# Kernel tuning notes

Measured on AMD Instinct MI355X. Metric: run time of the kernel, lower is better.

## Reference

```python
import jax, jax.numpy as jnp
import numpy as np

B, DIM, H, HD, DS = 256, 1024, 16, 64, 4
NL, NKV = HD, HD * DS  # mask shape constraint: num_tok_q == head_dim, num_tok_kv == head_dim*downscaling
EPS = 1e-5


def _ln(t, g, b):
    m = t.mean(-1, keepdims=True)
    v = ((t - m) ** 2).mean(-1, keepdims=True)
    return (t - m) / jnp.sqrt(v + EPS) * g + b


def setup_inputs() -> dict:
    key = jax.random.key(0)
    ks = jax.random.split(key, 7)
    s = DIM ** -0.5
    return {
        'x': jax.random.normal(ks[0], (B, NKV, DIM), jnp.float32),
        'latents': jax.random.normal(ks[1], (B, NL, DIM), jnp.float32),
        'Wq': jax.random.normal(ks[2], (DIM, DIM), jnp.float32) * s,
        'Wk': jax.random.normal(ks[3], (DIM, DIM), jnp.float32) * s,
        'Wv': jax.random.normal(ks[4], (DIM, DIM), jnp.float32) * s,
        'Wo': jax.random.normal(ks[5], (DIM, DIM), jnp.float32) * s,
        'bo': jnp.zeros((DIM,), jnp.float32),
        'g_out': jnp.ones((DIM,), jnp.float32),
        'b_out': jnp.zeros((DIM,), jnp.float32),
        'g_x': jnp.ones((DIM,), jnp.float32),
        'b_x': jnp.zeros((DIM,), jnp.float32),
        'g_l': jnp.ones((DIM,), jnp.float32),
        'b_l': jnp.zeros((DIM,), jnp.float32),
    }


def reference(x, latents, Wq, Wk, Wv, Wo, bo, g_out, b_out, g_x, b_x, g_l, b_l):
    # pre-norms
    ln_l = _ln(latents, g_l, b_l)   # (B, NL, DIM) -> queries
    ln_x = _ln(x, g_x, b_x)         # (B, NKV, DIM) -> keys/values
    # QKV projections (torch Linear: y = x @ W.T), split heads: b n (h d) -> b h n d
    q = (ln_l @ Wq.T).reshape(B, NL, H, HD).transpose(0, 2, 1, 3)
    k = (ln_x @ Wk.T).reshape(B, NKV, H, HD).transpose(0, 2, 1, 3)
    v = (ln_x @ Wv.T).reshape(B, NKV, H, HD).transpose(0, 2, 1, 3)
    qk = jnp.einsum('bhid,bhjd->bhij', q, k) * (HD ** -0.5)  # (B,H,NL,NKV)
    # faithful to original: (HD,HD) strict-upper -inf mask, repeat_interleave by DS along kv axis
    mask = jnp.triu(jnp.full((HD, HD), -jnp.inf, jnp.float32), k=1)
    mask = jnp.repeat(mask, DS, axis=1)  # (NL, NKV)
    attn = jax.nn.softmax(qk + mask[None, None], axis=-1)
    out = jnp.einsum('bhij,bhjd->bhid', attn, v)
    out = out.transpose(0, 2, 1, 3).reshape(B, NL, DIM)  # b h n d -> b n (h d)
    out = _ln(out, g_out, b_out)      # norm_out (hard-coded True)
    out = out @ Wo.T + bo             # to_out; dropout p=0 -> identity
    return latents + out              # residual=True
```

## Files before the change

### kernel.cpp

```cpp
#include <hip/hip_runtime.h>


typedef unsigned short u16;
typedef float f32x4 __attribute__((ext_vector_type(4)));
typedef short bf16x8 __attribute__((ext_vector_type(8)));
typedef u16 u16x4 __attribute__((ext_vector_type(4)));

#define DEV __device__ __forceinline__

DEV u16 f2bf(float f) {
  union { float f; unsigned int u; } c; c.f = f;
  unsigned int u = c.u;
  u += 0x7fffu + ((u >> 16) & 1u);
  return (u16)(u >> 16);
}
DEV float bf2f(u16 u) {
  union { unsigned int u; float f; } c; c.u = ((unsigned int)u) << 16; return c.f;
}
DEV f32x4 mfma16(bf16x8 a, bf16x8 b, f32x4 c) {
  return __builtin_amdgcn_mfma_f32_16x16x32_bf16(a, b, c, 0, 0, 0);
}
DEV void gl16(const void* g, void* l) {
  __builtin_amdgcn_global_load_lds((const __attribute__((address_space(1))) void*)g,
                                   (__attribute__((address_space(3))) void*)l, 16, 0, 0);
}

template<int INBF>
__global__ __launch_bounds__(256) void ln_kernel(const void* __restrict__ src,
                                                 const float* __restrict__ g,
                                                 const float* __restrict__ bta,
                                                 u16* __restrict__ dst) {
  const int row = blockIdx.x, tid = threadIdx.x;
  float v[4];
  if constexpr (INBF) {
    const u16x4 r = *((const u16x4*)((const u16*)src + (size_t)row * 1024) + tid);
#pragma unroll
    for (int i = 0; i < 4; ++i) v[i] = bf2f(r[i]);
  } else {
    const float4 r = *((const float4*)((const float*)src + (size_t)row * 1024) + tid);
    v[0] = r.x; v[1] = r.y; v[2] = r.z; v[3] = r.w;
  }
  float s = v[0] + v[1] + v[2] + v[3];
  float q = v[0]*v[0] + v[1]*v[1] + v[2]*v[2] + v[3]*v[3];
#pragma unroll
  for (int off = 32; off; off >>= 1) {
    s += __shfl_xor(s, off, 64);
    q += __shfl_xor(q, off, 64);
  }
  __shared__ float red[8];
  if ((tid & 63) == 0) { red[(tid >> 6) * 2] = s; red[(tid >> 6) * 2 + 1] = q; }
  __syncthreads();
  s = red[0] + red[2] + red[4] + red[6];
  q = red[1] + red[3] + red[5] + red[7];
  const float mean = s * (1.f / 1024.f);
  const float rstd = rsqrtf(q * (1.f / 1024.f) - mean * mean + 1e-5f);
  const float4 gv = *((const float4*)g + tid);
  const float4 bv = *((const float4*)bta + tid);
  u16x4 o;
  o[0] = f2bf((v[0] - mean) * rstd * gv.x + bv.x);
  o[1] = f2bf((v[1] - mean) * rstd * gv.y + bv.y);
  o[2] = f2bf((v[2] - mean) * rstd * gv.z + bv.z);
  o[3] = f2bf((v[3] - mean) * rstd * gv.w + bv.w);
  *((u16x4*)(dst + (size_t)row * 1024) + tid) = o;
}

__global__ __launch_bounds__(256) void cvt4_kernel(const float* __restrict__ w0,
                                                   const float* __restrict__ w1,
                                                   const float* __restrict__ w2,
                                                   const float* __restrict__ w3,
                                                   u16* __restrict__ out) {
  const int g = blockIdx.x >> 10;
  const float* src = (g == 0) ? w0 : (g == 1) ? w1 : (g == 2) ? w2 : w3;
  const int i = ((blockIdx.x & 1023) * 256 + threadIdx.x) * 4;
  const float4 v = *(const float4*)(src + i);
  u16x4 o; o[0] = f2bf(v.x); o[1] = f2bf(v.y); o[2] = f2bf(v.z); o[3] = f2bf(v.w);
  *(u16x4*)(out + (size_t)g * 1048576 + i) = o;
}

template<int MODE>
__global__ __launch_bounds__(512, 2) void gemm256(const u16* __restrict__ A,
                                                  const u16* __restrict__ B0,
                                                  const u16* __restrict__ B1,
                                                  u16* __restrict__ o0,
                                                  u16* __restrict__ o1,
                                                  const float* __restrict__ bias,
                                                  const float* __restrict__ resid,
                                                  float* __restrict__ outf,
                                                  int tiles_n) {
  constexpr int NT = 16;
  __shared__ u16 As[2][16384];
  __shared__ u16 Bs[2][16384];
  const int tid = threadIdx.x, lane = tid & 63, wid = tid >> 6;
  const int wm = wid >> 2, wn = wid & 3;
  const int q8 = (int)gridDim.x >> 3;
  const int wg = ((int)blockIdx.x & 7) * q8 + ((int)blockIdx.x >> 3);
  const int tn = wg % tiles_n, tm = wg / tiles_n;

  const u16* Asrc = A + (size_t)tm * 256 * 1024;
  const u16* Bsrc;
  if constexpr (MODE == 0)
    Bsrc = (tn < 4) ? (B0 + (size_t)tn * 256 * 1024) : (B1 + (size_t)(tn - 4) * 256 * 1024);
  else
    Bsrc = B0 + (size_t)tn * 256 * 1024;

  int goff[4], loff[4];
#pragma unroll
  for (int i = 0; i < 4; ++i) {
    const int s = i * 512 + tid;
    const int gr = s >> 3, gc = (s & 7) ^ (gr & 7);
    goff[i] = gr * 1024 + gc * 8;
    loff[i] = s * 8;
  }
  const int fr = lane & 15, fq = lane >> 4;
  int chk[2];
#pragma unroll
  for (int ks = 0; ks < 2; ++ks) chk[ks] = ((((ks << 2) + fq)) ^ (lane & 7)) * 8;

  f32x4 acc[8][4];
  const f32x4 z = {0.f, 0.f, 0.f, 0.f};
#pragma unroll
  for (int m = 0; m < 8; ++m)
#pragma unroll
    for (int n = 0; n < 4; ++n) acc[m][n] = z;

#define STG_A(buf, kt, h) { gl16(Asrc + (size_t)(kt) * 64 + goff[2*(h)],     &As[buf][loff[2*(h)]]); \
                            gl16(Asrc + (size_t)(kt) * 64 + goff[2*(h)+1],   &As[buf][loff[2*(h)+1]]); }
#define STG_B(buf, kt, h) { gl16(Bsrc + (size_t)(kt) * 64 + goff[2*(h)],     &Bs[buf][loff[2*(h)]]); \
                            gl16(Bsrc + (size_t)(kt) * 64 + goff[2*(h)+1],   &Bs[buf][loff[2*(h)+1]]); }
#define LDA(H) _Pragma("unroll") for (int mp = 0; mp < 4; ++mp) \
               _Pragma("unroll") for (int ks = 0; ks < 2; ++ks) \
                 af[mp][ks] = *(const bf16x8*)&Ab[(wm * 128 + ((H)*4 + mp) * 16 + fr) * 64 + chk[ks]];
#define LDB(DST, G) _Pragma("unroll") for (int np = 0; np < 2; ++np) \
                    _Pragma("unroll") for (int ks = 0; ks < 2; ++ks) \
                      DST[np][ks] = *(const bf16x8*)&Bb[(wn * 64 + ((G)*2 + np) * 16 + fr) * 64 + chk[ks]];
#define MFMA_Q(H, BF, G) _Pragma("unroll") for (int mp = 0; mp < 4; ++mp) \
                         _Pragma("unroll") for (int np = 0; np < 2; ++np) \
                         _Pragma("unroll") for (int ks = 0; ks < 2; ++ks) \
                           acc[(H)*4 + mp][(G)*2 + np] = mfma16(af[mp][ks], BF[np][ks], acc[(H)*4 + mp][(G)*2 + np]);

  STG_A(0, 0, 0); STG_A(0, 0, 1);
  STG_B(0, 0, 0); STG_B(0, 0, 1);
  STG_A(1, 1, 0); STG_A(1, 1, 1);
  asm volatile("s_waitcnt vmcnt(4)" ::: "memory");
  __builtin_amdgcn_s_barrier();

  for (int t = 0; t < NT; ++t) {
    const int bsel = t & 1;
    const u16* Ab = As[bsel];
    const u16* Bb = Bs[bsel];
    bf16x8 af[4][2], bfrA[2][2], bfrB[2][2];
    LDA(0); LDB(bfrA, 0);
    if (t + 1 < NT) STG_B(bsel ^ 1, t + 1, 0);
    __builtin_amdgcn_s_barrier();
    asm volatile("s_waitcnt lgkmcnt(0)" ::: "memory");
    __builtin_amdgcn_s_setprio(1);
    MFMA_Q(0, bfrA, 0);
    __builtin_amdgcn_s_setprio(0);
    __builtin_amdgcn_s_barrier();
    LDB(bfrB, 1);
    if (t + 1 < NT) STG_B(bsel ^ 1, t + 1, 1);
    __builtin_amdgcn_s_barrier();
    asm volatile("s_waitcnt lgkmcnt(0)" ::: "memory");
    __builtin_amdgcn_s_setprio(1);
    MFMA_Q(0, bfrB, 1);
    __builtin_amdgcn_s_setprio(0);
    __builtin_amdgcn_s_barrier();
    LDA(1);
    __builtin_amdgcn_s_barrier();
    asm volatile("s_waitcnt lgkmcnt(0)" ::: "memory");
    __builtin_amdgcn_s_setprio(1);
    MFMA_Q(1, bfrB, 1);
    __builtin_amdgcn_s_setprio(0);
    __builtin_amdgcn_s_barrier();
    if (t + 2 < NT) { STG_A(bsel, t + 2, 0); STG_A(bsel, t + 2, 1); }
    __builtin_amdgcn_s_setprio(1);
    MFMA_Q(1, bfrA, 0);
    __builtin_amdgcn_s_setprio(0);
    if (t + 2 < NT) asm volatile("s_waitcnt vmcnt(4)" ::: "memory");
    else            asm volatile("s_waitcnt vmcnt(0)" ::: "memory");
    __builtin_amdgcn_s_barrier();
  }
#undef STG_A
#undef STG_B
#undef LDA
#undef LDB
#undef MFMA_Q

  if constexpr (MODE == 0) {
    if (tn < 4) {
#pragma unroll
      for (int m = 0; m < 8; ++m) {
        const int t0 = wm * 128 + m * 16 + fq * 4;
#pragma unroll
        for (int n = 0; n < 4; ++n) {
          const int c = tn * 256 + wn * 64 + n * 16 + fr;
          const int h = c >> 6, d = c & 63;
          u16* p = o0 + ((size_t)(tm * 16 + h) * 256 + t0) * 64 + d;
#pragma unroll
          for (int j = 0; j < 4; ++j) p[j * 64] = f2bf(acc[m][n][j]);
        }
      }
    } else {
#pragma unroll
      for (int m = 0; m < 8; ++m) {
        const int t0 = wm * 128 + m * 16 + fq * 4;
#pragma unroll
        for (int n = 0; n < 4; ++n) {
          const int c = (tn - 4) * 256 + wn * 64 + n * 16 + fr;
          const int h = c >> 6, d = c & 63;
          u16x4 o;
#pragma unroll
          for (int j = 0; j < 4; ++j) o[j] = f2bf(acc[m][n][j]);
          *(u16x4*)(o1 + ((size_t)(tm * 16 + h) * 64 + d) * 256 + t0) = o;
        }
      }
    }
  } else if constexpr (MODE == 1) {
#pragma unroll
    for (int m = 0; m < 8; ++m) {
      const int r0 = tm * 256 + wm * 128 + m * 16 + fq * 4;
      const int b = r0 >> 6, i0 = r0 & 63;
#pragma unroll
      for (int n = 0; n < 4; ++n) {
        const int c = tn * 256 + wn * 64 + n * 16 + fr;
        const int h = c >> 6, d = c & 63;
        u16* p = o0 + ((size_t)(b * 16 + h) * 64 + i0) * 64 + d;
#pragma unroll
        for (int j = 0; j < 4; ++j) p[j * 64] = f2bf(acc[m][n][j]);
      }
    }
  } else {
#pragma unroll
    for (int m = 0; m < 8; ++m) {
      const int r0 = tm * 256 + wm * 128 + m * 16 + fq * 4;
#pragma unroll
      for (int n = 0; n < 4; ++n) {
        const int c = tn * 256 + wn * 64 + n * 16 + fr;
        const float bc = bias[c];
#pragma unroll
        for (int j = 0; j < 4; ++j) {
          const size_t idx = (size_t)(r0 + j) * 1024 + c;
          outf[idx] = acc[m][n][j] + bc + resid[idx];
        }
      }
    }
  }
}

__global__ __launch_bounds__(256) void attn_kernel(const u16* __restrict__ Qb,
                                                   const u16* __restrict__ Kb,
                                                   const u16* __restrict__ Vt,
                                                   u16* __restrict__ AO) {
  __shared__ u16 Qs[64 * 64];
  __shared__ u16 Ks[256 * 64];
  __shared__ u16 Vs[64 * 256];
  const int bh = blockIdx.x;
  const int tid = threadIdx.x, lane = tid & 63, wv = tid >> 6;
  const u16* qsrc = Qb + (size_t)bh * 4096;
  const u16* ksrc = Kb + (size_t)bh * 16384;
  const u16* vsrc = Vt + (size_t)bh * 16384;
#pragma unroll
  for (int i = 0; i < 2; ++i) gl16(qsrc + (i * 256 + tid) * 8, &Qs[(i * 256 + tid) * 8]);
#pragma unroll
  for (int i = 0; i < 8; ++i) gl16(ksrc + (i * 256 + tid) * 8, &Ks[(i * 256 + tid) * 8]);
#pragma unroll
  for (int i = 0; i < 8; ++i) gl16(vsrc + (i * 256 + tid) * 8, &Vs[(i * 256 + tid) * 8]);
  __syncthreads();

  f32x4 sacc[16];
  const f32x4 z = {0.f, 0.f, 0.f, 0.f};
#pragma unroll
  for (int n = 0; n < 16; ++n) sacc[n] = z;
#pragma unroll
  for (int s = 0; s < 2; ++s) {
    const bf16x8 aq = *(const bf16x8*)&Qs[(wv * 16 + (lane & 15)) * 64 + s * 32 + (lane >> 4) * 8];
#pragma unroll
    for (int n = 0; n < 16; ++n) {
      const bf16x8 bk = *(const bf16x8*)&Ks[(n * 16 + (lane & 15)) * 64 + s * 32 + (lane >> 4) * 8];
      sacc[n] = mfma16(aq, bk, sacc[n]);
    }
  }

  const int rgrp = lane >> 4, cl = lane & 15;
#pragma unroll
  for (int j = 0; j < 4; ++j) {
    const int qrow = (wv << 4) + (rgrp << 2) + j;
    float m_ = -1e30f;
#pragma unroll
    for (int n = 0; n < 16; ++n) {
      const int col = (n << 4) + cl;
      float sv = sacc[n][j] * 0.125f;
      sv = ((col >> 2) <= qrow) ? sv : -1e30f;
      sacc[n][j] = sv;
      m_ = fmaxf(m_, sv);
    }
#pragma unroll
    for (int off = 8; off; off >>= 1) m_ = fmaxf(m_, __shfl_xor(m_, off, 64));
    float s_ = 0.f;
#pragma unroll
    for (int n = 0; n < 16; ++n) {
      const float p = exp2f((sacc[n][j] - m_) * 1.44269504f);
      sacc[n][j] = p;
      s_ += p;
    }
#pragma unroll
    for (int off = 8; off; off >>= 1) s_ += __shfl_xor(s_, off, 64);
    const float inv = 1.0f / s_;
#pragma unroll
    for (int n = 0; n < 16; ++n) sacc[n][j] *= inv;
  }

  __syncthreads();
  u16* Ps = Ks;
#pragma unroll
  for (int n = 0; n < 16; ++n)
#pragma unroll
    for (int j = 0; j < 4; ++j)
      Ps[((wv << 4) + (rgrp << 2) + j) * 256 + (n << 4) + cl] = f2bf(sacc[n][j]);
  __syncthreads();

  f32x4 oacc[4];
#pragma unroll
  for (int n = 0; n < 4; ++n) oacc[n] = z;
#pragma unroll
  for (int ks = 0; ks < 8; ++ks) {
    const bf16x8 ap = *(const bf16x8*)&Ps[(wv * 16 + (lane & 15)) * 256 + ks * 32 + (lane >> 4) * 8];
#pragma unroll
    for (int n = 0; n < 4; ++n) {
      const bf16x8 bv = *(const bf16x8*)&Vs[(n * 16 + (lane & 15)) * 256 + ks * 32 + (lane >> 4) * 8];
      oacc[n] = mfma16(ap, bv, oacc[n]);
    }
  }
  const int b = bh >> 4, h = bh & 15;
  u16* obase = AO + (size_t)b * 65536 + (size_t)h * 64;
#pragma unroll
  for (int n = 0; n < 4; ++n)
#pragma unroll
    for (int j = 0; j < 4; ++j) {
      const int qrow = (wv << 4) + (rgrp << 2) + j;
      const int d = (n << 4) + cl;
      obase[(size_t)qrow * 1024 + d] = f2bf(oacc[n][j]);
    }
}

extern "C" void kernel_launch(void* const* d_in, const int* in_sizes, int n_in,
                              void* d_out, int out_size, void* d_ws, size_t ws_size,
                              hipStream_t stream) {
  const float* x     = (const float*)d_in[0];
  const float* lat   = (const float*)d_in[1];
  const float* Wq    = (const float*)d_in[2];
  const float* Wk    = (const float*)d_in[3];
  const float* Wv    = (const float*)d_in[4];
  const float* Wo    = (const float*)d_in[5];
  const float* bo    = (const float*)d_in[6];
  const float* g_out = (const float*)d_in[7];
  const float* b_out = (const float*)d_in[8];
  const float* g_x   = (const float*)d_in[9];
  const float* b_x   = (const float*)d_in[10];
  const float* g_l   = (const float*)d_in[11];
  const float* b_l   = (const float*)d_in[12];
  float* out = (float*)d_out;

  char* W = (char*)d_ws;
  u16* wqb = (u16*)(W + 0);
  u16* wkb = (u16*)(W + 2097152);
  u16* wvb = (u16*)(W + 4194304);
  u16* wob = (u16*)(W + 6291456);
  u16* lnl = (u16*)(W + 8388608);
  u16* lnx = (u16*)(W + 41943040);
  u16* qb  = (u16*)(W + 176160768);
  u16* kb  = (u16*)(W + 209715200);
  u16* vt  = (u16*)(W + 343932928);
  u16* ao  = lnx;
  u16* lna = qb;

  cvt4_kernel<<<4096, 256, 0, stream>>>(Wq, Wk, Wv, Wo, wqb);

  ln_kernel<0><<<16384, 256, 0, stream>>>(lat, g_l, b_l, lnl);
  ln_kernel<0><<<65536, 256, 0, stream>>>(x, g_x, b_x, lnx);

  gemm256<0><<<256 * 8, 512, 0, stream>>>(lnx, wkb, wvb, kb, vt, nullptr, nullptr, nullptr, 8);
  gemm256<1><<<64 * 4, 512, 0, stream>>>(lnl, wqb, nullptr, qb, nullptr, nullptr, nullptr, nullptr, 4);

  attn_kernel<<<4096, 256, 0, stream>>>(qb, kb, vt, ao);

  ln_kernel<1><<<16384, 256, 0, stream>>>(ao, g_out, b_out, lna);

  gemm256<2><<<64 * 4, 512, 0, stream>>>(lna, wob, nullptr, nullptr, nullptr, bo, lat, out, 4);
}
```

Before: 649.3 us.

## Replace interleaved 8-wave GEMM schedule with simple double-buffered tile loop

```diff
diff --git a/kernel.cpp b/kernel.cpp
--- a/kernel.cpp
+++ b/kernel.cpp
@@ -123,68 +123,49 @@
 #pragma unroll
     for (int n = 0; n < 4; ++n) acc[m][n] = z;
 
-#define STG_A(buf, kt, h) { gl16(Asrc + (size_t)(kt) * 64 + goff[2*(h)],     &As[buf][loff[2*(h)]]); \
-                            gl16(Asrc + (size_t)(kt) * 64 + goff[2*(h)+1],   &As[buf][loff[2*(h)+1]]); }
-#define STG_B(buf, kt, h) { gl16(Bsrc + (size_t)(kt) * 64 + goff[2*(h)],     &Bs[buf][loff[2*(h)]]); \
-                            gl16(Bsrc + (size_t)(kt) * 64 + goff[2*(h)+1],   &Bs[buf][loff[2*(h)+1]]); }
-#define LDA(H) _Pragma("unroll") for (int mp = 0; mp < 4; ++mp) \
-               _Pragma("unroll") for (int ks = 0; ks < 2; ++ks) \
-                 af[mp][ks] = *(const bf16x8*)&Ab[(wm * 128 + ((H)*4 + mp) * 16 + fr) * 64 + chk[ks]];
-#define LDB(DST, G) _Pragma("unroll") for (int np = 0; np < 2; ++np) \
-                    _Pragma("unroll") for (int ks = 0; ks < 2; ++ks) \
-                      DST[np][ks] = *(const bf16x8*)&Bb[(wn * 64 + ((G)*2 + np) * 16 + fr) * 64 + chk[ks]];
-#define MFMA_Q(H, BF, G) _Pragma("unroll") for (int mp = 0; mp < 4; ++mp) \
-                         _Pragma("unroll") for (int np = 0; np < 2; ++np) \
-                         _Pragma("unroll") for (int ks = 0; ks < 2; ++ks) \
-                           acc[(H)*4 + mp][(G)*2 + np] = mfma16(af[mp][ks], BF[np][ks], acc[(H)*4 + mp][(G)*2 + np]);
-
-  STG_A(0, 0, 0); STG_A(0, 0, 1);
-  STG_B(0, 0, 0); STG_B(0, 0, 1);
-  STG_A(1, 1, 0); STG_A(1, 1, 1);
-  asm volatile("s_waitcnt vmcnt(4)" ::: "memory");
+#define STG_TILE(buf, kt) { \
+    gl16(Asrc + (size_t)(kt) * 64 + goff[0], &As[buf][loff[0]]); \
+    gl16(Asrc + (size_t)(kt) * 64 + goff[1], &As[buf][loff[1]]); \
+    gl16(Asrc + (size_t)(kt) * 64 + goff[2], &As[buf][loff[2]]); \
+    gl16(Asrc + (size_t)(kt) * 64 + goff[3], &As[buf][loff[3]]); \
+    gl16(Bsrc + (size_t)(kt) * 64 + goff[0], &Bs[buf][loff[0]]); \
+    gl16(Bsrc + (size_t)(kt) * 64 + goff[1], &Bs[buf][loff[1]]); \
+    gl16(Bsrc + (size_t)(kt) * 64 + goff[2], &Bs[buf][loff[2]]); \
+    gl16(Bsrc + (size_t)(kt) * 64 + goff[3], &Bs[buf][loff[3]]); }
+
+  STG_TILE(0, 0);
+  asm volatile("s_waitcnt vmcnt(0)" ::: "memory");
   __builtin_amdgcn_s_barrier();
 
   for (int t = 0; t < NT; ++t) {
     const int bsel = t & 1;
     const u16* Ab = As[bsel];
     const u16* Bb = Bs[bsel];
-    bf16x8 af[4][2], bfrA[2][2], bfrB[2][2];
-    LDA(0); LDB(bfrA, 0);
-    if (t + 1 < NT) STG_B(bsel ^ 1, t + 1, 0);
+    if (t + 1 < NT) STG_TILE(bsel ^ 1, t + 1);
+    bf16x8 af[8][2], bfr[4][2];
+#pragma unroll
+    for (int m = 0; m < 8; ++m)
+#pragma unroll
+      for (int ks = 0; ks < 2; ++ks)
+        af[m][ks] = *(const bf16x8*)&Ab[(wm * 128 + m * 16 + fr) * 64 + chk[ks]];
+#pragma unroll
+    for (int n = 0; n < 4; ++n)
+#pragma unroll
+      for (int ks = 0; ks < 2; ++ks)
+        bfr[n][ks] = *(const bf16x8*)&Bb[(wn * 64 + n * 16 + fr) * 64 + chk[ks]];
+    __builtin_amdgcn_s_setprio(1);
+#pragma unroll
+    for (int m = 0; m < 8; ++m)
+#pragma unroll
+      for (int n = 0; n < 4; ++n)
+#pragma unroll
+        for (int ks = 0; ks < 2; ++ks)
+          acc[m][n] = mfma16(af[m][ks], bfr[n][ks], acc[m][n]);
+    __builtin_amdgcn_s_setprio(0);
+    asm volatile("s_waitcnt vmcnt(0)" ::: "memory");
     __builtin_amdgcn_s_barrier();
-    asm volatile("s_waitcnt lgkmcnt(0)" ::: "memory");
-    __builtin_amdgcn_s_setprio(1);
-    MFMA_Q(0, bfrA, 0);
-    __builtin_amdgcn_s_setprio(0);
-    __builtin_amdgcn_s_barrier();
-    LDB(bfrB, 1);
-    if (t + 1 < NT) STG_B(bsel ^ 1, t + 1, 1);
-    __builtin_amdgcn_s_barrier();
-    asm volatile("s_waitcnt lgkmcnt(0)" ::: "memory");
-    __builtin_amdgcn_s_setprio(1);
-    MFMA_Q(0, bfrB, 1);
-    __builtin_amdgcn_s_setprio(0);
-    __builtin_amdgcn_s_barrier();
-    LDA(1);
-    __builtin_amdgcn_s_barrier();
-    asm volatile("s_waitcnt lgkmcnt(0)" ::: "memory");
-    __builtin_amdgcn_s_setprio(1);
-    MFMA_Q(1, bfrB, 1);
-    __builtin_amdgcn_s_setprio(0);
-    __builtin_amdgcn_s_barrier();
-    if (t + 2 < NT) { STG_A(bsel, t + 2, 0); STG_A(bsel, t + 2, 1); }
-    __builtin_amdgcn_s_setprio(1);
-    MFMA_Q(1, bfrA, 0);
-    __builtin_amdgcn_s_setprio(0);
-    if (t + 2 < NT) asm volatile("s_waitcnt vmcnt(4)" ::: "memory");
-    else            asm volatile("s_waitcnt vmcnt(0)" ::: "memory");
-    __builtin_amdgcn_s_barrier();
-  }
-#undef STG_A
-#undef STG_B
-#undef LDA
-#undef LDB
-#undef MFMA_Q
+  }
+#undef STG_TILE
 
   if constexpr (MODE == 0) {
     if (tn < 4) {
```

New measurement: 680.0 us. +4.7%, slower.

## Merge weight-convert and layernorm launches, fuse Q into KV GEMM, defer softmax normalization

Applied to the files above, without the earlier changes.

```diff
diff --git a/kernel.cpp b/kernel.cpp
--- a/kernel.cpp
+++ b/kernel.cpp
@@ -25,21 +25,74 @@
                                    (__attribute__((address_space(3))) void*)l, 16, 0, 0);
 }
 
-template<int INBF>
-__global__ __launch_bounds__(256) void ln_kernel(const void* __restrict__ src,
-                                                 const float* __restrict__ g,
-                                                 const float* __restrict__ bta,
-                                                 u16* __restrict__ dst) {
+DEV void ln_row_f32(const float* __restrict__ srcrow, const float* __restrict__ g,
+                    const float* __restrict__ bta, u16* __restrict__ dstrow,
+                    int tid, float* red) {
+  const float4 r = *((const float4*)srcrow + tid);
+  float v[4] = {r.x, r.y, r.z, r.w};
+  float s = v[0] + v[1] + v[2] + v[3];
+  float q = v[0]*v[0] + v[1]*v[1] + v[2]*v[2] + v[3]*v[3];
+#pragma unroll
+  for (int off = 32; off; off >>= 1) {
+    s += __shfl_xor(s, off, 64);
+    q += __shfl_xor(q, off, 64);
+  }
+  if ((tid & 63) == 0) { red[(tid >> 6) * 2] = s; red[(tid >> 6) * 2 + 1] = q; }
+  __syncthreads();
+  s = red[0] + red[2] + red[4] + red[6];
+  q = red[1] + red[3] + red[5] + red[7];
+  const float mean = s * (1.f / 1024.f);
+  const float rstd = rsqrtf(q * (1.f / 1024.f) - mean * mean + 1e-5f);
+  const float4 gv = *((const float4*)g + tid);
+  const float4 bv = *((const float4*)bta + tid);
+  u16x4 o;
+  o[0] = f2bf((v[0] - mean) * rstd * gv.x + bv.x);
+  o[1] = f2bf((v[1] - mean) * rstd * gv.y + bv.y);
+  o[2] = f2bf((v[2] - mean) * rstd * gv.z + bv.z);
+  o[3] = f2bf((v[3] - mean) * rstd * gv.w + bv.w);
+  *((u16x4*)dstrow + tid) = o;
+}
+
+__global__ __launch_bounds__(256) void fused_pre(const float* __restrict__ w0,
+                                                 const float* __restrict__ w1,
+                                                 const float* __restrict__ w2,
+                                                 const float* __restrict__ w3,
+                                                 u16* __restrict__ wout,
+                                                 const float* __restrict__ lat,
+                                                 const float* __restrict__ g_l,
+                                                 const float* __restrict__ b_l,
+                                                 u16* __restrict__ lnl,
+                                                 const float* __restrict__ x,
+                                                 const float* __restrict__ g_x,
+                                                 const float* __restrict__ b_x,
+                                                 u16* __restrict__ lnx) {
+  __shared__ float red[8];
+  const int bid = blockIdx.x, tid = threadIdx.x;
+  if (bid < 4096) {
+    const int g = bid >> 10;
+    const float* src = (g == 0) ? w0 : (g == 1) ? w1 : (g == 2) ? w2 : w3;
+    const int i = ((bid & 1023) * 256 + tid) * 4;
+    const float4 v = *(const float4*)(src + i);
+    u16x4 o; o[0] = f2bf(v.x); o[1] = f2bf(v.y); o[2] = f2bf(v.z); o[3] = f2bf(v.w);
+    *(u16x4*)(wout + (size_t)g * 1048576 + i) = o;
+  } else if (bid < 20480) {
+    const int row = bid - 4096;
+    ln_row_f32(lat + (size_t)row * 1024, g_l, b_l, lnl + (size_t)row * 1024, tid, red);
+  } else {
+    const int row = bid - 20480;
+    ln_row_f32(x + (size_t)row * 1024, g_x, b_x, lnx + (size_t)row * 1024, tid, red);
+  }
+}
+
+__global__ __launch_bounds__(256) void ln_bf(const u16* __restrict__ src,
+                                             const float* __restrict__ g,
+                                             const float* __restrict__ bta,
+                                             u16* __restrict__ dst) {
   const int row = blockIdx.x, tid = threadIdx.x;
+  const u16x4 r = *((const u16x4*)(src + (size_t)row * 1024) + tid);
   float v[4];
-  if constexpr (INBF) {
-    const u16x4 r = *((const u16x4*)((const u16*)src + (size_t)row * 1024) + tid);
-#pragma unroll
-    for (int i = 0; i < 4; ++i) v[i] = bf2f(r[i]);
-  } else {
-    const float4 r = *((const float4*)((const float*)src + (size_t)row * 1024) + tid);
-    v[0] = r.x; v[1] = r.y; v[2] = r.z; v[3] = r.w;
-  }
+#pragma unroll
+  for (int i = 0; i < 4; ++i) v[i] = bf2f(r[i]);
   float s = v[0] + v[1] + v[2] + v[3];
   float q = v[0]*v[0] + v[1]*v[1] + v[2]*v[2] + v[3]*v[3];
 #pragma unroll
@@ -64,64 +117,11 @@
   *((u16x4*)(dst + (size_t)row * 1024) + tid) = o;
 }
 
-__global__ __launch_bounds__(256) void cvt4_kernel(const float* __restrict__ w0,
-                                                   const float* __restrict__ w1,
-                                                   const float* __restrict__ w2,
-                                                   const float* __restrict__ w3,
-                                                   u16* __restrict__ out) {
-  const int g = blockIdx.x >> 10;
-  const float* src = (g == 0) ? w0 : (g == 1) ? w1 : (g == 2) ? w2 : w3;
-  const int i = ((blockIdx.x & 1023) * 256 + threadIdx.x) * 4;
-  const float4 v = *(const float4*)(src + i);
-  u16x4 o; o[0] = f2bf(v.x); o[1] = f2bf(v.y); o[2] = f2bf(v.z); o[3] = f2bf(v.w);
-  *(u16x4*)(out + (size_t)g * 1048576 + i) = o;
-}
-
-template<int MODE>
-__global__ __launch_bounds__(512, 2) void gemm256(const u16* __restrict__ A,
-                                                  const u16* __restrict__ B0,
-                                                  const u16* __restrict__ B1,
-                                                  u16* __restrict__ o0,
-                                                  u16* __restrict__ o1,
-                                                  const float* __restrict__ bias,
-                                                  const float* __restrict__ resid,
-                                                  float* __restrict__ outf,
-                                                  int tiles_n) {
+DEV void gemm_core(const u16* __restrict__ Asrc, const u16* __restrict__ Bsrc,
+                   u16 (&As)[2][16384], u16 (&Bs)[2][16384],
+                   const int (&goff)[4], const int (&loff)[4], const int (&chk)[2],
+                   int wm, int wn, int fr, f32x4 (&acc)[8][4]) {
   constexpr int NT = 16;
-  __shared__ u16 As[2][16384];
-  __shared__ u16 Bs[2][16384];
-  const int tid = threadIdx.x, lane = tid & 63, wid = tid >> 6;
-  const int wm = wid >> 2, wn = wid & 3;
-  const int q8 = (int)gridDim.x >> 3;
-  const int wg = ((int)blockIdx.x & 7) * q8 + ((int)blockIdx.x >> 3);
-  const int tn = wg % tiles_n, tm = wg / tiles_n;
-
-  const u16* Asrc = A + (size_t)tm * 256 * 1024;
-  const u16* Bsrc;
-  if constexpr (MODE == 0)
-    Bsrc = (tn < 4) ? (B0 + (size_t)tn * 256 * 1024) : (B1 + (size_t)(tn - 4) * 256 * 1024);
-  else
-    Bsrc = B0 + (size_t)tn * 256 * 1024;
-
-  int goff[4], loff[4];
-#pragma unroll
-  for (int i = 0; i < 4; ++i) {
-    const int s = i * 512 + tid;
-    const int gr = s >> 3, gc = (s & 7) ^ (gr & 7);
-    goff[i] = gr * 1024 + gc * 8;
-    loff[i] = s * 8;
-  }
-  const int fr = lane & 15, fq = lane >> 4;
-  int chk[2];
-#pragma unroll
-  for (int ks = 0; ks < 2; ++ks) chk[ks] = ((((ks << 2) + fq)) ^ (lane & 7)) * 8;
-
-  f32x4 acc[8][4];
-  const f32x4 z = {0.f, 0.f, 0.f, 0.f};
-#pragma unroll
-  for (int m = 0; m < 8; ++m)
-#pragma unroll
-    for (int n = 0; n < 4; ++n) acc[m][n] = z;
 
 #define STG_A(buf, kt, h) { gl16(Asrc + (size_t)(kt) * 64 + goff[2*(h)],     &As[buf][loff[2*(h)]]); \
                             gl16(Asrc + (size_t)(kt) * 64 + goff[2*(h)+1],   &As[buf][loff[2*(h)+1]]); }
@@ -185,37 +185,55 @@
 #undef LDA
 #undef LDB
 #undef MFMA_Q
-
-  if constexpr (MODE == 0) {
-    if (tn < 4) {
-#pragma unroll
-      for (int m = 0; m < 8; ++m) {
-        const int t0 = wm * 128 + m * 16 + fq * 4;
-#pragma unroll
-        for (int n = 0; n < 4; ++n) {
-          const int c = tn * 256 + wn * 64 + n * 16 + fr;
-          const int h = c >> 6, d = c & 63;
-          u16* p = o0 + ((size_t)(tm * 16 + h) * 256 + t0) * 64 + d;
-#pragma unroll
-          for (int j = 0; j < 4; ++j) p[j * 64] = f2bf(acc[m][n][j]);
-        }
-      }
-    } else {
-#pragma unroll
-      for (int m = 0; m < 8; ++m) {
-        const int t0 = wm * 128 + m * 16 + fq * 4;
-#pragma unroll
-        for (int n = 0; n < 4; ++n) {
-          const int c = (tn - 4) * 256 + wn * 64 + n * 16 + fr;
-          const int h = c >> 6, d = c & 63;
-          u16x4 o;
-#pragma unroll
-          for (int j = 0; j < 4; ++j) o[j] = f2bf(acc[m][n][j]);
-          *(u16x4*)(o1 + ((size_t)(tm * 16 + h) * 64 + d) * 256 + t0) = o;
-        }
-      }
-    }
-  } else if constexpr (MODE == 1) {
+}
+
+DEV void gemm_prep(int tid, int lane, int (&goff)[4], int (&loff)[4], int (&chk)[2],
+                   f32x4 (&acc)[8][4]) {
+#pragma unroll
+  for (int i = 0; i < 4; ++i) {
+    const int s = i * 512 + tid;
+    const int gr = s >> 3, gc = (s & 7) ^ (gr & 7);
+    goff[i] = gr * 1024 + gc * 8;
+    loff[i] = s * 8;
+  }
+  const int fq = lane >> 4;
+#pragma unroll
+  for (int ks = 0; ks < 2; ++ks) chk[ks] = ((((ks << 2) + fq)) ^ (lane & 7)) * 8;
+  const f32x4 z = {0.f, 0.f, 0.f, 0.f};
+#pragma unroll
+  for (int m = 0; m < 8; ++m)
+#pragma unroll
+    for (int n = 0; n < 4; ++n) acc[m][n] = z;
+}
+
+__global__ __launch_bounds__(512, 2) void gemm_qkv(const u16* __restrict__ A0,
+                                                   const u16* __restrict__ A1,
+                                                   const u16* __restrict__ Bkv,
+                                                   const u16* __restrict__ Bq,
+                                                   u16* __restrict__ kb,
+                                                   u16* __restrict__ vt,
+                                                   u16* __restrict__ qb) {
+  __shared__ u16 As[2][16384];
+  __shared__ u16 Bs[2][16384];
+  const int tid = threadIdx.x, lane = tid & 63, wid = tid >> 6;
+  const int wm = wid >> 2, wn = wid & 3;
+  const int q8 = (int)gridDim.x >> 3;
+  const int wg = ((int)blockIdx.x & 7) * q8 + ((int)blockIdx.x >> 3);
+  const bool isQ = wg >= 2048;
+  const int wg0 = isQ ? wg - 2048 : wg;
+  const int tiles_n = isQ ? 4 : 8;
+  const int tn = wg0 % tiles_n, tm = wg0 / tiles_n;
+
+  const u16* Asrc = (isQ ? A1 : A0) + (size_t)tm * 262144;
+  const u16* Bsrc = (isQ ? Bq : Bkv) + (size_t)tn * 262144;
+
+  int goff[4], loff[4], chk[2];
+  f32x4 acc[8][4];
+  gemm_prep(tid, lane, goff, loff, chk, acc);
+  gemm_core(Asrc, Bsrc, As, Bs, goff, loff, chk, wm, wn, lane & 15, acc);
+
+  const int fr = lane & 15, fq = lane >> 4;
+  if (isQ) {
 #pragma unroll
     for (int m = 0; m < 8; ++m) {
       const int r0 = tm * 256 + wm * 128 + m * 16 + fq * 4;
@@ -224,24 +242,74 @@
       for (int n = 0; n < 4; ++n) {
         const int c = tn * 256 + wn * 64 + n * 16 + fr;
         const int h = c >> 6, d = c & 63;
-        u16* p = o0 + ((size_t)(b * 16 + h) * 64 + i0) * 64 + d;
+        u16* p = qb + ((size_t)(b * 16 + h) * 64 + i0) * 64 + d;
 #pragma unroll
         for (int j = 0; j < 4; ++j) p[j * 64] = f2bf(acc[m][n][j]);
       }
     }
-  } else {
+  } else if (tn < 4) {
 #pragma unroll
     for (int m = 0; m < 8; ++m) {
-      const int r0 = tm * 256 + wm * 128 + m * 16 + fq * 4;
+      const int t0 = wm * 128 + m * 16 + fq * 4;
 #pragma unroll
       for (int n = 0; n < 4; ++n) {
         const int c = tn * 256 + wn * 64 + n * 16 + fr;
-        const float bc = bias[c];
-#pragma unroll
-        for (int j = 0; j < 4; ++j) {
-          const size_t idx = (size_t)(r0 + j) * 1024 + c;
-          outf[idx] = acc[m][n][j] + bc + resid[idx];
-        }
+        const int h = c >> 6, d = c & 63;
+        u16* p = kb + ((size_t)(tm * 16 + h) * 256 + t0) * 64 + d;
+#pragma unroll
+        for (int j = 0; j < 4; ++j) p[j * 64] = f2bf(acc[m][n][j]);
+      }
+    }
+  } else {
+#pragma unroll
+    for (int m = 0; m < 8; ++m) {
+      const int t0 = wm * 128 + m * 16 + fq * 4;
+#pragma unroll
+      for (int n = 0; n < 4; ++n) {
+        const int c = (tn - 4) * 256 + wn * 64 + n * 16 + fr;
+        const int h = c >> 6, d = c & 63;
+        u16x4 o;
+#pragma unroll
+        for (int j = 0; j < 4; ++j) o[j] = f2bf(acc[m][n][j]);
+        *(u16x4*)(vt + ((size_t)(tm * 16 + h) * 64 + d) * 256 + t0) = o;
+      }
+    }
+  }
+}
+
+__global__ __launch_bounds__(512, 2) void gemm_out(const u16* __restrict__ A,
+                                                   const u16* __restrict__ Bo,
+                                                   const float* __restrict__ bias,
+                                                   const float* __restrict__ resid,
+                                                   float* __restrict__ outf) {
+  __shared__ u16 As[2][16384];
+  __shared__ u16 Bs[2][16384];
+  const int tid = threadIdx.x, lane = tid & 63, wid = tid >> 6;
+  const int wm = wid >> 2, wn = wid & 3;
+  const int q8 = (int)gridDim.x >> 3;
+  const int wg = ((int)blockIdx.x & 7) * q8 + ((int)blockIdx.x >> 3);
+  const int tn = wg % 4, tm = wg / 4;
+
+  const u16* Asrc = A + (size_t)tm * 262144;
+  const u16* Bsrc = Bo + (size_t)tn * 262144;
+
+  int goff[4], loff[4], chk[2];
+  f32x4 acc[8][4];
+  gemm_prep(tid, lane, goff, loff, chk, acc);
+  gemm_core(Asrc, Bsrc, As, Bs, goff, loff, chk, wm, wn, lane & 15, acc);
+
+  const int fr = lane & 15, fq = lane >> 4;
+#pragma unroll
+  for (int m = 0; m < 8; ++m) {
+    const int r0 = tm * 256 + wm * 128 + m * 16 + fq * 4;
+#pragma unroll
+    for (int n = 0; n < 4; ++n) {
+      const int c = tn * 256 + wn * 64 + n * 16 + fr;
+      const float bc = bias[c];
+#pragma unroll
+      for (int j = 0; j < 4; ++j) {
+        const size_t idx = (size_t)(r0 + j) * 1024 + c;
+        outf[idx] = acc[m][n][j] + bc + resid[idx];
       }
     }
   }
@@ -265,7 +333,8 @@
   for (int i = 0; i < 8; ++i) gl16(ksrc + (i * 256 + tid) * 8, &Ks[(i * 256 + tid) * 8]);
 #pragma unroll
   for (int i = 0; i < 8; ++i) gl16(vsrc + (i * 256 + tid) * 8, &Vs[(i * 256 + tid) * 8]);
-  __syncthreads();
+  asm volatile("s_waitcnt vmcnt(8)" ::: "memory");
+  __builtin_amdgcn_s_barrier();
 
   f32x4 sacc[16];
   const f32x4 z = {0.f, 0.f, 0.f, 0.f};
@@ -282,6 +351,7 @@
   }
 
   const int rgrp = lane >> 4, cl = lane & 15;
+  float inv[4];
 #pragma unroll
   for (int j = 0; j < 4; ++j) {
     const int qrow = (wv << 4) + (rgrp << 2) + j;
@@ -305,12 +375,11 @@
     }
 #pragma unroll
     for (int off = 8; off; off >>= 1) s_ += __shfl_xor(s_, off, 64);
-    const float inv = 1.0f / s_;
-#pragma unroll
-    for (int n = 0; n < 16; ++n) sacc[n][j] *= inv;
-  }
-
-  __syncthreads();
+    inv[j] = 1.0f / s_;
+  }
+
+  asm volatile("s_waitcnt vmcnt(0)" ::: "memory");
+  __builtin_amdgcn_s_barrier();
   u16* Ps = Ks;
 #pragma unroll
   for (int n = 0; n < 16; ++n)
@@ -339,7 +408,7 @@
     for (int j = 0; j < 4; ++j) {
       const int qrow = (wv << 4) + (rgrp << 2) + j;
       const int d = (n << 4) + cl;
-      obase[(size_t)qrow * 1024 + d] = f2bf(oacc[n][j]);
+      obase[(size_t)qrow * 1024 + d] = f2bf(oacc[n][j] * inv[j]);
     }
 }
 
@@ -373,18 +442,17 @@
   u16* vt  = (u16*)(W + 343932928);
   u16* ao  = lnx;
   u16* lna = qb;
-
-  cvt4_kernel<<<4096, 256, 0, stream>>>(Wq, Wk, Wv, Wo, wqb);
-
-  ln_kernel<0><<<16384, 256, 0, stream>>>(lat, g_l, b_l, lnl);
-  ln_kernel<0><<<65536, 256, 0, stream>>>(x, g_x, b_x, lnx);
-
-  gemm256<0><<<256 * 8, 512, 0, stream>>>(lnx, wkb, wvb, kb, vt, nullptr, nullptr, nullptr, 8);
-  gemm256<1><<<64 * 4, 512, 0, stream>>>(lnl, wqb, nullptr, qb, nullptr, nullptr, nullptr, nullptr, 4);
+  (void)wvb;
+
+  fused_pre<<<86016, 256, 0, stream>>>(Wq, Wk, Wv, Wo, wqb,
+                                       lat, g_l, b_l, lnl,
+                                       x, g_x, b_x, lnx);
+
+  gemm_qkv<<<2304, 512, 0, stream>>>(lnx, lnl, wkb, wqb, kb, vt, qb);
 
   attn_kernel<<<4096, 256, 0, stream>>>(qb, kb, vt, ao);
 
-  ln_kernel<1><<<16384, 256, 0, stream>>>(ao, g_out, b_out, lna);
-
-  gemm256<2><<<64 * 4, 512, 0, stream>>>(lna, wob, nullptr, nullptr, nullptr, bo, lat, out, 4);
-}
+  ln_bf<<<16384, 256, 0, stream>>>(ao, g_out, b_out, lna);
+
+  gemm_out<<<256, 512, 0, stream>>>(lna, wob, bo, lat, out);
+}
```

New measurement: 623.7 us (median of 2 runs). 3.9% less time.
